# Optimization experiments

Hardware: AMD Instinct MI355X
Metric: run time of the kernel (lower is better)

Reference implementation:

```python
import jax, jax.numpy as jnp
import numpy as np

B, U, T, H, D, K = 8, 512, 1024, 512, 128, 10

def setup_inputs() -> dict:
    key = jax.random.key(0)
    k1, k2, k3 = jax.random.split(key, 3)
    h_t = jax.random.normal(k1, (B, U, H), dtype=jnp.float32)
    ctx = jax.random.normal(k2, (B, T, D), dtype=jnp.float32)
    mask = jnp.ones((B, T), dtype=jnp.float32)
    # small init scale so exp(linear(h_t)) stays numerically tame
    W = jax.random.normal(k3, (H, 3 * K), dtype=jnp.float32) * 0.02
    b = jnp.zeros((3 * K,), dtype=jnp.float32)
    return {"h_t": h_t, "ctx": ctx, "mask": mask, "W": W, "b": b}

def reference(h_t, ctx, mask, W, b):
    # params = exp(Linear(h_t)) : [B, U, 3K]
    p = jnp.exp(h_t @ W + b)
    alpha, beta, kappa = jnp.split(p, 3, axis=-1)  # each [B, U, K]
    kappa = jnp.cumsum(kappa * 0.2, axis=1)        # monotone attention position
    u = jnp.arange(ctx.shape[1], dtype=jnp.float32)  # [T]
    # phi[b,u,t] = sum_k alpha * exp(-beta * (kappa - t)^2)
    diff = kappa[:, :, None, :] - u[None, None, :, None]          # [B, U, T, K]
    phi = jnp.sum(alpha[:, :, None, :] * jnp.exp(-beta[:, :, None, :] * diff * diff), axis=-1)  # [B, U, T]
    # masked weighted sum over ctx positions
    out = jnp.einsum('but,btd,bt->bud', phi, ctx, mask)           # [B, U, D]
    return out
```

## Files before the change

kernel.cpp:

```cpp
#include <hip/hip_runtime.h>
#include <math.h>

#define B_ 8
#define U_ 512
#define T_ 1024
#define H_ 512
#define D_ 128
#define K_ 10

#define UT 8
#define TC 32
#define NTILES 64

typedef __attribute__((ext_vector_type(8))) short bf16x8;
typedef __attribute__((ext_vector_type(4))) float f32x4;

__device__ __forceinline__ unsigned short f32_to_bf16_rtne(float f) {
    unsigned u = __float_as_uint(f);
    unsigned r = u + 0x7FFFu + ((u >> 16) & 1u);
    return (unsigned short)(r >> 16);
}
__device__ __forceinline__ unsigned pack_bf16(float a, float b) {
    return (unsigned)f32_to_bf16_rtne(a) | ((unsigned)f32_to_bf16_rtne(b) << 16);
}

__device__ __forceinline__ unsigned long long pack_flag(float v) {
    unsigned lo = __float_as_uint(v);
    return ((unsigned long long)(lo ^ 0x80000000u) << 32) | lo;
}
__device__ __forceinline__ bool unpack_flag(unsigned long long g, float* v) {
    unsigned lo = (unsigned)g, hi = (unsigned)(g >> 32);
    *v = __uint_as_float(lo);
    return (hi == (lo ^ 0x80000000u)) && (*v > 0.f);
}

__global__ __launch_bounds__(256, 2)
void fused_kernel(const float* __restrict__ h_t,
                  const float* __restrict__ ctx,
                  const float* __restrict__ mask,
                  const float* __restrict__ W,
                  const float* __restrict__ bias,
                  float* __restrict__ out,
                  unsigned long long* __restrict__ Tg) {
    __shared__ unsigned short A_s[16 * 512];
    __shared__ float Cp[2][8][33];
    __shared__ float ab_s[8][20];
    __shared__ float kin_s[8][K_];
    __shared__ float L_s[8][K_];
    __shared__ float part_s[16][K_];
    __shared__ float pre_s[K_];
    __shared__ float phi_s[8][TC + 4];
    __shared__ float ctx_s[TC][D_];
    __shared__ float red_lo[80], red_hi[80];

    int tid = threadIdx.x;
    int lane = tid & 63;
    int w = tid >> 6;
    int b = blockIdx.x >> 6;
    int mytile = blockIdx.x & 63;
    int row0 = b * U_ + mytile * UT;

    int khalf = w >> 1;
    int ntile = w & 1;
    int c = 16 * ntile + (lane & 15);
    int kb = khalf * 256 + ((lane >> 4) << 3);
    bf16x8 bfrag[8];
    #pragma unroll
    for (int s = 0; s < 8; ++s) {
        #pragma unroll
        for (int e = 0; e < 8; ++e) {
            float wv = (c < 30) ? W[(size_t)(kb + 32 * s + e) * 30 + c] : 0.f;
            bfrag[s][e] = (short)f32_to_bf16_rtne(wv);
        }
    }

    {
        int r = tid >> 5;
        int kc = (tid & 31) * 16;
        const float4* src = (const float4*)(h_t + (size_t)(row0 + r) * H_ + kc);
        unsigned pk[8];
        #pragma unroll
        for (int i = 0; i < 4; ++i) {
            float4 v = src[i];
            pk[2 * i]     = pack_bf16(v.x, v.y);
            pk[2 * i + 1] = pack_bf16(v.z, v.w);
        }
        int base = r * 1024 + kc * 2;
        int swz = (r & 7) << 4;
        *(int4*)((char*)A_s + ((base) ^ swz)) =
            make_int4((int)pk[0], (int)pk[1], (int)pk[2], (int)pk[3]);
        *(int4*)((char*)A_s + ((base + 16) ^ swz)) =
            make_int4((int)pk[4], (int)pk[5], (int)pk[6], (int)pk[7]);
    }
    __syncthreads();

    {
        int ar = lane & 15;
        int abase = ar * 1024 + (khalf * 256 + ((lane >> 4) << 3)) * 2;
        int aswz = (ar & 7) << 4;
        f32x4 acc = {0.f, 0.f, 0.f, 0.f};
        #pragma unroll
        for (int s = 0; s < 8; ++s) {
            bf16x8 af = *(const bf16x8*)((const char*)A_s + ((abase + s * 64) ^ aswz));
            acc = __builtin_amdgcn_mfma_f32_16x16x32_bf16(af, bfrag[s], acc, 0, 0, 0);
        }
        int rbase = (lane >> 4) * 4;
        if (rbase < 8) {
            int ccol = 16 * ntile + (lane & 15);
            #pragma unroll
            for (int r = 0; r < 4; ++r)
                Cp[khalf][rbase + r][ccol] = acc[r];
        }
    }
    __syncthreads();

    if (tid < 240) {
        int rr = tid / 30, cc = tid % 30;
        float p = __expf(Cp[0][rr][cc] + Cp[1][rr][cc] + bias[cc]);
        if (cc < 20) ab_s[rr][cc] = p;
        else         kin_s[rr][cc - 20] = 0.2f * p;
    }
    __syncthreads();

    if (tid < UT * K_) {
        int u_l = tid / K_, k = tid % K_;
        float ssum = 0.f;
        for (int r = 0; r <= u_l; ++r) ssum += kin_s[r][k];
        L_s[u_l][k] = ssum;
        if (u_l == UT - 1)
            __hip_atomic_store(&Tg[((size_t)b * NTILES + mytile) * K_ + k],
                               pack_flag(ssum),
                               __ATOMIC_RELAXED, __HIP_MEMORY_SCOPE_AGENT);
    } else if (tid < 240) {
        int o = tid - 80;
        part_s[o / K_][o % K_] = 0.f;
    }
    __syncthreads();

    if (tid < 160) {
        int jg = tid / K_, k = tid % K_;
        const unsigned long long* tp = &Tg[((size_t)b * NTILES) * K_ + k];
        float vals[4];
        bool rdy[4] = {true, true, true, true};
        int js[4];
        int cnt = 0;
        for (int j = jg; j < mytile; j += 16) { js[cnt] = j; rdy[cnt] = false; vals[cnt] = 0.f; ++cnt; }
        for (;;) {
            bool all_ready = true;
            #pragma unroll
            for (int i = 0; i < 4; ++i) {
                if (i < cnt && !rdy[i]) {
                    unsigned long long g = __hip_atomic_load(tp + (size_t)js[i] * K_,
                                                             __ATOMIC_RELAXED, __HIP_MEMORY_SCOPE_AGENT);
                    float v;
                    if (unpack_flag(g, &v)) { vals[i] = v; rdy[i] = true; }
                    else all_ready = false;
                }
            }
            if (all_ready) break;
            __builtin_amdgcn_s_sleep(1);
        }
        float sum = 0.f;
        #pragma unroll
        for (int i = 0; i < 4; ++i) if (i < cnt) sum += vals[i];
        part_s[jg][k] = sum;
    }
    __syncthreads();
    if (tid < K_) {
        float pre = 0.f;
        #pragma unroll
        for (int jg = 0; jg < 16; ++jg) pre += part_s[jg][tid];
        pre_s[tid] = pre;
    }
    __syncthreads();

    if (tid < UT * K_) {
        int u_l = tid / K_, k = tid % K_;
        float kv = pre_s[k] + L_s[u_l][k];
        kin_s[u_l][k] = kv;
        float bvv = ab_s[u_l][10 + k];
        float r = sqrtf(20.f / bvv);
        red_lo[tid] = kv - r; red_hi[tid] = kv + r;
    }
    __syncthreads();
    if (tid < 64) {
        float l = red_lo[tid], h = red_hi[tid];
        if (tid < 16) { l = fminf(l, red_lo[tid + 64]); h = fmaxf(h, red_hi[tid + 64]); }
        #pragma unroll
        for (int d = 32; d > 0; d >>= 1) {
            l = fminf(l, __shfl_xor(l, d, 64));
            h = fmaxf(h, __shfl_xor(h, d, 64));
        }
        if (tid == 0) { red_lo[0] = l; red_hi[0] = h; }
    }
    __syncthreads();
    int t_begin = max(0, (int)floorf(red_lo[0]));
    int t_end   = min(T_, (int)ceilf(red_hi[0]) + 1);

    int u_l = tid >> 5;
    int g   = tid & 31;
    float acc4[4] = {0.f, 0.f, 0.f, 0.f};

    for (int t0 = t_begin; t0 < t_end; t0 += TC) {
        __syncthreads();
        {
            #pragma unroll
            for (int i = 0; i < (TC * D_ / 4) / 256; ++i) {
                int slot = tid + 256 * i;
                int r = slot >> 5;
                int rc = min(t0 + r, T_ - 1);
                const float4* src = (const float4*)(ctx + ((size_t)b * T_ + rc) * D_);
                ((float4*)(&ctx_s[0][0]))[slot] = src[slot & 31];
            }
        }
        {
            int uu = tid >> 5;
            int tl = tid & 31;
            int tf_i = t0 + tl;
            float tf = (float)tf_i;
            float ph = 0.f;
            #pragma unroll
            for (int k = 0; k < K_; ++k) {
                float d = kin_s[uu][k] - tf;
                float x = ab_s[uu][10 + k] * d * d;
                ph += ab_s[uu][k] * __expf(-x);
            }
            int tm = min(tf_i, T_ - 1);
            ph = (tf_i < T_) ? ph * mask[(size_t)b * T_ + tm] : 0.f;
            phi_s[uu][tl] = ph;
        }
        __syncthreads();
        for (int tl4 = 0; tl4 < TC / 4; ++tl4) {
            float4 ph4 = *(const float4*)(&phi_s[u_l][4 * tl4]);
            #pragma unroll
            for (int qq = 0; qq < 4; ++qq) {
                float ph = (qq == 0) ? ph4.x : (qq == 1) ? ph4.y : (qq == 2) ? ph4.z : ph4.w;
                float4 c0 = ((const float4*)(&ctx_s[4 * tl4 + qq][0]))[g];
                acc4[0] += ph * c0.x; acc4[1] += ph * c0.y;
                acc4[2] += ph * c0.z; acc4[3] += ph * c0.w;
            }
        }
    }

    float* orow = out + ((size_t)(b * U_ + mytile * UT) + u_l) * D_;
    *(float4*)(orow + 4 * g) = make_float4(acc4[0], acc4[1], acc4[2], acc4[3]);
}

extern "C" void kernel_launch(void* const* d_in, const int* in_sizes, int n_in,
                              void* d_out, int out_size, void* d_ws, size_t ws_size,
                              hipStream_t stream) {
    const float* h_t  = (const float*)d_in[0];
    const float* ctx  = (const float*)d_in[1];
    const float* mask = (const float*)d_in[2];
    const float* W    = (const float*)d_in[3];
    const float* bias = (const float*)d_in[4];
    float* out = (float*)d_out;
    unsigned long long* Tg = (unsigned long long*)d_ws;

    fused_kernel<<<dim3(B_ * NTILES), dim3(256), 0, stream>>>(
        h_t, ctx, mask, W, bias, out, Tg);
}
```

Baseline: 15.50 us.

## Double rows per block to 16 and split the GEMV K-dim four ways

Each block now covers 16 U-rows with 512 threads, so the grid is half as large (256 blocks). The h_t projection splits K across four wave pairs instead of two. The cross-block cumulative-sum wait shrinks to 32 predecessor tiles, each polled by one thread. In the weighted sum over ctx, half the threads each accumulate two rows, so each ctx tile in shared memory serves twice as many outputs. In exchange, each block's t-window grows, since it must cover the kappa range of 16 rows, and half the threads sit idle during the accumulation loop.

```diff
diff --git a/kernel.cpp b/kernel.cpp
--- a/kernel.cpp
+++ b/kernel.cpp
@@ -8,9 +8,9 @@
 #define D_ 128
 #define K_ 10
 
-#define UT 8
+#define UT 16
 #define TC 32
-#define NTILES 64
+#define NT2 32
 
 typedef __attribute__((ext_vector_type(8))) short bf16x8;
 typedef __attribute__((ext_vector_type(4))) float f32x4;
@@ -34,7 +34,7 @@
     return (hi == (lo ^ 0x80000000u)) && (*v > 0.f);
 }
 
-__global__ __launch_bounds__(256, 2)
+__global__ __launch_bounds__(512, 1)
 void fused_kernel(const float* __restrict__ h_t,
                   const float* __restrict__ ctx,
                   const float* __restrict__ mask,
@@ -43,30 +43,30 @@
                   float* __restrict__ out,
                   unsigned long long* __restrict__ Tg) {
     __shared__ unsigned short A_s[16 * 512];
-    __shared__ float Cp[2][8][33];
-    __shared__ float ab_s[8][20];
-    __shared__ float kin_s[8][K_];
-    __shared__ float L_s[8][K_];
-    __shared__ float part_s[16][K_];
+    __shared__ float Cp[4][16][33];
+    __shared__ float ab_s[16][20];
+    __shared__ float kin_s[16][K_];
+    __shared__ float L_s[16][K_];
+    __shared__ float part_s[NT2][K_];
     __shared__ float pre_s[K_];
-    __shared__ float phi_s[8][TC + 4];
+    __shared__ float phi_s[16][TC + 4];
     __shared__ float ctx_s[TC][D_];
-    __shared__ float red_lo[80], red_hi[80];
+    __shared__ float red_lo[160], red_hi[160];
 
     int tid = threadIdx.x;
     int lane = tid & 63;
     int w = tid >> 6;
-    int b = blockIdx.x >> 6;
-    int mytile = blockIdx.x & 63;
+    int b = blockIdx.x >> 5;
+    int mytile = blockIdx.x & 31;
     int row0 = b * U_ + mytile * UT;
 
-    int khalf = w >> 1;
+    int kq = w >> 1;
     int ntile = w & 1;
     int c = 16 * ntile + (lane & 15);
-    int kb = khalf * 256 + ((lane >> 4) << 3);
-    bf16x8 bfrag[8];
+    int kb = kq * 128 + ((lane >> 4) << 3);
+    bf16x8 bfrag[4];
     #pragma unroll
-    for (int s = 0; s < 8; ++s) {
+    for (int s = 0; s < 4; ++s) {
         #pragma unroll
         for (int e = 0; e < 8; ++e) {
             float wv = (c < 30) ? W[(size_t)(kb + 32 * s + e) * 30 + c] : 0.f;
@@ -96,27 +96,26 @@
 
     {
         int ar = lane & 15;
-        int abase = ar * 1024 + (khalf * 256 + ((lane >> 4) << 3)) * 2;
+        int abase = ar * 1024 + (kq * 128 + ((lane >> 4) << 3)) * 2;
         int aswz = (ar & 7) << 4;
         f32x4 acc = {0.f, 0.f, 0.f, 0.f};
         #pragma unroll
-        for (int s = 0; s < 8; ++s) {
+        for (int s = 0; s < 4; ++s) {
             bf16x8 af = *(const bf16x8*)((const char*)A_s + ((abase + s * 64) ^ aswz));
             acc = __builtin_amdgcn_mfma_f32_16x16x32_bf16(af, bfrag[s], acc, 0, 0, 0);
         }
         int rbase = (lane >> 4) * 4;
-        if (rbase < 8) {
-            int ccol = 16 * ntile + (lane & 15);
-            #pragma unroll
-            for (int r = 0; r < 4; ++r)
-                Cp[khalf][rbase + r][ccol] = acc[r];
-        }
-    }
-    __syncthreads();
-
-    if (tid < 240) {
+        int ccol = 16 * ntile + (lane & 15);
+        #pragma unroll
+        for (int r = 0; r < 4; ++r)
+            Cp[kq][rbase + r][ccol] = acc[r];
+    }
+    __syncthreads();
+
+    if (tid < 480) {
         int rr = tid / 30, cc = tid % 30;
-        float p = __expf(Cp[0][rr][cc] + Cp[1][rr][cc] + bias[cc]);
+        float dot = (Cp[0][rr][cc] + Cp[1][rr][cc]) + (Cp[2][rr][cc] + Cp[3][rr][cc]);
+        float p = __expf(dot + bias[cc]);
         if (cc < 20) ab_s[rr][cc] = p;
         else         kin_s[rr][cc - 20] = 0.2f * p;
     }
@@ -128,48 +127,31 @@
         for (int r = 0; r <= u_l; ++r) ssum += kin_s[r][k];
         L_s[u_l][k] = ssum;
         if (u_l == UT - 1)
-            __hip_atomic_store(&Tg[((size_t)b * NTILES + mytile) * K_ + k],
+            __hip_atomic_store(&Tg[((size_t)b * NT2 + mytile) * K_ + k],
                                pack_flag(ssum),
                                __ATOMIC_RELAXED, __HIP_MEMORY_SCOPE_AGENT);
-    } else if (tid < 240) {
-        int o = tid - 80;
-        part_s[o / K_][o % K_] = 0.f;
-    }
-    __syncthreads();
-
-    if (tid < 160) {
+    }
+    __syncthreads();
+
+    if (tid < NT2 * K_) {
         int jg = tid / K_, k = tid % K_;
-        const unsigned long long* tp = &Tg[((size_t)b * NTILES) * K_ + k];
-        float vals[4];
-        bool rdy[4] = {true, true, true, true};
-        int js[4];
-        int cnt = 0;
-        for (int j = jg; j < mytile; j += 16) { js[cnt] = j; rdy[cnt] = false; vals[cnt] = 0.f; ++cnt; }
-        for (;;) {
-            bool all_ready = true;
-            #pragma unroll
-            for (int i = 0; i < 4; ++i) {
-                if (i < cnt && !rdy[i]) {
-                    unsigned long long g = __hip_atomic_load(tp + (size_t)js[i] * K_,
-                                                             __ATOMIC_RELAXED, __HIP_MEMORY_SCOPE_AGENT);
-                    float v;
-                    if (unpack_flag(g, &v)) { vals[i] = v; rdy[i] = true; }
-                    else all_ready = false;
-                }
-            }
-            if (all_ready) break;
-            __builtin_amdgcn_s_sleep(1);
-        }
-        float sum = 0.f;
-        #pragma unroll
-        for (int i = 0; i < 4; ++i) if (i < cnt) sum += vals[i];
-        part_s[jg][k] = sum;
+        float v = 0.f;
+        if (jg < mytile) {
+            const unsigned long long* p = &Tg[((size_t)b * NT2 + jg) * K_ + k];
+            for (;;) {
+                unsigned long long g = __hip_atomic_load(p, __ATOMIC_RELAXED,
+                                                         __HIP_MEMORY_SCOPE_AGENT);
+                if (unpack_flag(g, &v)) break;
+                __builtin_amdgcn_s_sleep(1);
+            }
+        }
+        part_s[jg][k] = v;
     }
     __syncthreads();
     if (tid < K_) {
         float pre = 0.f;
         #pragma unroll
-        for (int jg = 0; jg < 16; ++jg) pre += part_s[jg][tid];
+        for (int jg = 0; jg < NT2; ++jg) pre += part_s[jg][tid];
         pre_s[tid] = pre;
     }
     __syncthreads();
@@ -184,8 +166,9 @@
     }
     __syncthreads();
     if (tid < 64) {
-        float l = red_lo[tid], h = red_hi[tid];
-        if (tid < 16) { l = fminf(l, red_lo[tid + 64]); h = fmaxf(h, red_hi[tid + 64]); }
+        float l = fminf(red_lo[tid], red_lo[tid + 64]);
+        float h = fmaxf(red_hi[tid], red_hi[tid + 64]);
+        if (tid < 32) { l = fminf(l, red_lo[tid + 128]); h = fmaxf(h, red_hi[tid + 128]); }
         #pragma unroll
         for (int d = 32; d > 0; d >>= 1) {
             l = fminf(l, __shfl_xor(l, d, 64));
@@ -197,16 +180,17 @@
     int t_begin = max(0, (int)floorf(red_lo[0]));
     int t_end   = min(T_, (int)ceilf(red_hi[0]) + 1);
 
-    int u_l = tid >> 5;
-    int g   = tid & 31;
-    float acc4[4] = {0.f, 0.f, 0.f, 0.f};
+    int u2 = tid >> 5;
+    int g  = tid & 31;
+    float a0[4] = {0.f, 0.f, 0.f, 0.f};
+    float a1[4] = {0.f, 0.f, 0.f, 0.f};
 
     for (int t0 = t_begin; t0 < t_end; t0 += TC) {
         __syncthreads();
         {
             #pragma unroll
-            for (int i = 0; i < (TC * D_ / 4) / 256; ++i) {
-                int slot = tid + 256 * i;
+            for (int i = 0; i < (TC * D_ / 4) / 512; ++i) {
+                int slot = tid + 512 * i;
                 int r = slot >> 5;
                 int rc = min(t0 + r, T_ - 1);
                 const float4* src = (const float4*)(ctx + ((size_t)b * T_ + rc) * D_);
@@ -230,20 +214,30 @@
             phi_s[uu][tl] = ph;
         }
         __syncthreads();
-        for (int tl4 = 0; tl4 < TC / 4; ++tl4) {
-            float4 ph4 = *(const float4*)(&phi_s[u_l][4 * tl4]);
-            #pragma unroll
-            for (int qq = 0; qq < 4; ++qq) {
-                float ph = (qq == 0) ? ph4.x : (qq == 1) ? ph4.y : (qq == 2) ? ph4.z : ph4.w;
-                float4 c0 = ((const float4*)(&ctx_s[4 * tl4 + qq][0]))[g];
-                acc4[0] += ph * c0.x; acc4[1] += ph * c0.y;
-                acc4[2] += ph * c0.z; acc4[3] += ph * c0.w;
-            }
-        }
-    }
-
-    float* orow = out + ((size_t)(b * U_ + mytile * UT) + u_l) * D_;
-    *(float4*)(orow + 4 * g) = make_float4(acc4[0], acc4[1], acc4[2], acc4[3]);
+        if (tid < 256) {
+            for (int tl4 = 0; tl4 < TC / 4; ++tl4) {
+                float4 p0 = *(const float4*)(&phi_s[u2][4 * tl4]);
+                float4 p1 = *(const float4*)(&phi_s[u2 + 8][4 * tl4]);
+                #pragma unroll
+                for (int qq = 0; qq < 4; ++qq) {
+                    float f0 = (qq == 0) ? p0.x : (qq == 1) ? p0.y : (qq == 2) ? p0.z : p0.w;
+                    float f1 = (qq == 0) ? p1.x : (qq == 1) ? p1.y : (qq == 2) ? p1.z : p1.w;
+                    float4 c0 = ((const float4*)(&ctx_s[4 * tl4 + qq][0]))[g];
+                    a0[0] += f0 * c0.x; a0[1] += f0 * c0.y;
+                    a0[2] += f0 * c0.z; a0[3] += f0 * c0.w;
+                    a1[0] += f1 * c0.x; a1[1] += f1 * c0.y;
+                    a1[2] += f1 * c0.z; a1[3] += f1 * c0.w;
+                }
+            }
+        }
+    }
+
+    if (tid < 256) {
+        float* orow0 = out + ((size_t)(b * U_ + mytile * UT) + u2) * D_;
+        float* orow1 = out + ((size_t)(b * U_ + mytile * UT) + u2 + 8) * D_;
+        *(float4*)(orow0 + 4 * g) = make_float4(a0[0], a0[1], a0[2], a0[3]);
+        *(float4*)(orow1 + 4 * g) = make_float4(a1[0], a1[1], a1[2], a1[3]);
+    }
 }
 
 extern "C" void kernel_launch(void* const* d_in, const int* in_sizes, int n_in,
@@ -257,6 +251,6 @@
     float* out = (float*)d_out;
     unsigned long long* Tg = (unsigned long long*)d_ws;
 
-    fused_kernel<<<dim3(B_ * NTILES), dim3(256), 0, stream>>>(
+    fused_kernel<<<dim3(B_ * NT2), dim3(512), 0, stream>>>(
         h_t, ctx, mask, W, bias, out, Tg);
 }
```

Result: faster. 13.04 us, median of 2 (-15.9%).
